# Kernel tuning notes

Hardware: AMD Instinct MI355X
Metric: run time of the kernel (lower is better)

## Reference

```python
import jax, jax.numpy as jnp
import numpy as np

N = 50000
E = 800000
NEG_SLOPE = 0.2
BN_EPS = 1e-5


def _gat_conv(x, src, dst, W, a_src, a_dst, bias, heads, out_ch, concat):
    # Linear projection per head: [N, heads, out_ch]
    h = (x @ W).reshape(-1, heads, out_ch)
    # Per-node attention terms alpha_src/alpha_dst: [N, heads]
    al_s = (h * a_src[None]).sum(-1)
    al_d = (h * a_dst[None]).sum(-1)
    # Edge logits with LeakyReLU: [E, heads]
    logits = jax.nn.leaky_relu(al_s[src] + al_d[dst], NEG_SLOPE)
    # Segment (scatter) softmax over edges grouped by destination node
    m = jax.ops.segment_max(logits, dst, num_segments=N)
    e = jnp.exp(logits - m[dst])
    s = jax.ops.segment_sum(e, dst, num_segments=N)
    alpha = e / (s[dst] + 1e-16)                      # [E, heads]
    # Weighted message aggregation: scatter-add to destinations
    msg = h[src] * alpha[:, :, None]                  # [E, heads, out_ch]
    out = jax.ops.segment_sum(msg, dst, num_segments=N)  # [N, heads, out_ch]
    out = out.reshape(-1, heads * out_ch) if concat else out.mean(axis=1)
    return out + bias


def _bn_eval(x, gamma, beta, mean, var):
    return (x - mean) * jax.lax.rsqrt(var + BN_EPS) * gamma + beta


def setup_inputs() -> dict:
    key = jax.random.key(0)
    ks = jax.random.split(key, 12)
    in_ch, hid, heads, out_cls = 128, 64, 2, 40
    return {
        "x": jax.random.normal(ks[0], (N, in_ch), jnp.float32),
        "edge_index": jax.random.randint(ks[1], (2, E), 0, N, jnp.int32),
        "W1": jax.random.normal(ks[2], (in_ch, heads * hid), jnp.float32) * 0.1,
        "a1_src": jax.random.normal(ks[3], (heads, hid), jnp.float32) * 0.1,
        "a1_dst": jax.random.normal(ks[4], (heads, hid), jnp.float32) * 0.1,
        "b1": jnp.zeros((heads * hid,), jnp.float32),
        "bn1_gamma": jnp.ones((heads * hid,), jnp.float32),
        "bn1_beta": jnp.zeros((heads * hid,), jnp.float32),
        "bn1_mean": jax.random.normal(ks[5], (heads * hid,), jnp.float32) * 0.1,
        "bn1_var": jax.random.uniform(ks[6], (heads * hid,), jnp.float32, 0.5, 1.5),
        "W2": jax.random.normal(ks[7], (heads * hid, out_cls), jnp.float32) * 0.1,
        "a2_src": jax.random.normal(ks[8], (1, out_cls), jnp.float32) * 0.1,
        "a2_dst": jax.random.normal(ks[9], (1, out_cls), jnp.float32) * 0.1,
        "b2": jnp.zeros((out_cls,), jnp.float32),
    }


def reference(x, edge_index, W1, a1_src, a1_dst, b1, bn1_gamma, bn1_beta,
              bn1_mean, bn1_var, W2, a2_src, a2_dst, b2):
    # add self loops
    loops = jnp.arange(N, dtype=edge_index.dtype)
    src = jnp.concatenate([edge_index[0], loops])
    dst = jnp.concatenate([edge_index[1], loops])
    # layer 1: GATConv(heads=2, concat) -> BN(eval) -> ReLU (dropout is eval no-op)
    h = _gat_conv(x, src, dst, W1, a1_src, a1_dst, b1, heads=2, out_ch=64, concat=True)
    h = jax.nn.relu(_bn_eval(h, bn1_gamma, bn1_beta, bn1_mean, bn1_var))
    # output layer: GATConv(heads=1, concat=False)
    out = _gat_conv(h, src, dst, W2, a2_src, a2_dst, b2, heads=1, out_ch=40, concat=False)
    return jax.nn.log_softmax(out, axis=1)
```

## Files before the change

kernel.cpp:

```cpp
#include <hip/hip_runtime.h>
#include <hip/hip_bf16.h>

#define NEG_SLOPE 0.2f
#define BN_EPS 1e-5f

#define NBLK 256
#define COARSE_SHIFT 9
#define COARSE_NPB 512

__device__ __forceinline__ float wred_sum(float v) {
    #pragma unroll
    for (int m = 32; m > 0; m >>= 1) v += __shfl_xor(v, m);
    return v;
}
__device__ __forceinline__ float wred_max(float v) {
    #pragma unroll
    for (int m = 32; m > 0; m >>= 1) v = fmaxf(v, __shfl_xor(v, m));
    return v;
}
__device__ __forceinline__ float xor16_sum(float v) {
    #pragma unroll
    for (int m = 1; m < 16; m <<= 1) v += __shfl_xor(v, m);
    return v;
}

__device__ __forceinline__ unsigned pack_bf16(float a, float b) {
    __hip_bfloat162 t;
    t.x = __float2bfloat16(a);
    t.y = __float2bfloat16(b);
    return *(unsigned*)&t;
}
__device__ __forceinline__ float2 unpack_bf16(unsigned u) {
    __hip_bfloat162 t = *(__hip_bfloat162*)&u;
    return {__bfloat162float(t.x), __bfloat162float(t.y)};
}

__device__ __forceinline__ unsigned enc_ord(float f) {
    unsigned u = __float_as_uint(f);
    return (u & 0x80000000u) ? ~u : (u | 0x80000000u);
}
__device__ __forceinline__ float dec_ord(unsigned e) {
    unsigned u = (e & 0x80000000u) ? (e ^ 0x80000000u) : ~e;
    return __uint_as_float(u);
}

__global__ __launch_bounds__(256) void part_hist(const int* __restrict__ ei, int E, int Et,
                                                 int chunk, int* __restrict__ hist, int nCoarse) {
    __shared__ int h[128];
    int b = blockIdx.x, t = threadIdx.x;
    if (t < 128) h[t] = 0;
    __syncthreads();
    int beg = b * chunk, end = min(beg + chunk, Et);
    for (int idx = beg + t; idx < end; idx += 256) {
        int d = (idx < E) ? ei[E + idx] : (idx - E);
        atomicAdd(&h[d >> COARSE_SHIFT], 1);
    }
    __syncthreads();
    if (t < nCoarse) hist[t * NBLK + b] = h[t];
}

__global__ __launch_bounds__(256) void coarse_total(const int* __restrict__ hist,
                                                    int* __restrict__ ctot) {
    __shared__ int red[256];
    int c = blockIdx.x, t = threadIdx.x;
    red[t] = hist[c * NBLK + t];
    __syncthreads();
    for (int off = 128; off > 0; off >>= 1) {
        if (t < off) red[t] += red[t + off];
        __syncthreads();
    }
    if (t == 0) ctot[c] = red[0];
}

__global__ __launch_bounds__(128) void coarse_scan(const int* __restrict__ ctot,
                                                   int* __restrict__ cbase, int nCoarse) {
    __shared__ int s[128];
    int t = threadIdx.x;
    int v = (t < nCoarse) ? ctot[t] : 0;
    s[t] = v;
    __syncthreads();
    for (int off = 1; off < 128; off <<= 1) {
        int u = (t >= off) ? s[t - off] : 0;
        __syncthreads();
        s[t] += u;
        __syncthreads();
    }
    if (t < nCoarse) cbase[t] = s[t] - v;
    if (t == 127) cbase[nCoarse] = s[127];
}

__global__ __launch_bounds__(64) void part_scan(int* __restrict__ hist,
                                                const int* __restrict__ cbase, int nCoarse) {
    int c = blockIdx.x, t = threadIdx.x;
    int base = cbase[c];
    int idx = c * NBLK + 4 * t;
    int4 v = *(int4*)&hist[idx];
    int sl = v.x + v.y + v.z + v.w;
    int inc = sl;
    #pragma unroll
    for (int off = 1; off < 64; off <<= 1) {
        int u = __shfl_up(inc, off);
        if (t >= off) inc += u;
    }
    int exc = inc - sl + base;
    int4 o;
    o.x = exc;
    o.y = exc + v.x;
    o.z = exc + v.x + v.y;
    o.w = exc + v.x + v.y + v.z;
    *(int4*)&hist[idx] = o;
}

__global__ __launch_bounds__(256) void part_scatter(const int* __restrict__ ei, int E, int Et,
                                                    int chunk, const int* __restrict__ hist,
                                                    unsigned* __restrict__ staged, int nCoarse) {
    __shared__ int cur[128];
    int b = blockIdx.x, t = threadIdx.x;
    if (t < nCoarse) cur[t] = hist[t * NBLK + b];
    __syncthreads();
    int beg = b * chunk, end = min(beg + chunk, Et);
    for (int idx = beg + t; idx < end; idx += 256) {
        int s, d;
        if (idx < E) { s = ei[idx]; d = ei[E + idx]; }
        else         { s = idx - E; d = idx - E; }
        int c = d >> COARSE_SHIFT;
        int pos = atomicAdd(&cur[c], 1);
        staged[pos] = ((unsigned)s << COARSE_SHIFT) | (unsigned)(d & (COARSE_NPB - 1));
    }
}

__global__ __launch_bounds__(512) void fine_place(const unsigned* __restrict__ staged,
                                                  const int* __restrict__ cbase,
                                                  int* __restrict__ offs,
                                                  int* __restrict__ csr, int Nn, int nCoarse) {
    __shared__ int hcnt[COARSE_NPB];
    __shared__ int scn[COARSE_NPB];
    int b = blockIdx.x, t = threadIdx.x;
    int node0 = b << COARSE_SHIFT;
    int nloc = min(COARSE_NPB, Nn - node0);
    hcnt[t] = 0;
    __syncthreads();
    int ebeg = cbase[b], eend = cbase[b + 1];
    for (int p = ebeg + t; p < eend; p += 512) {
        atomicAdd(&hcnt[staged[p] & (COARSE_NPB - 1)], 1);
    }
    __syncthreads();
    int val = hcnt[t];
    scn[t] = val;
    __syncthreads();
    for (int off = 1; off < COARSE_NPB; off <<= 1) {
        int u = (t >= off) ? scn[t - off] : 0;
        __syncthreads();
        scn[t] += u;
        __syncthreads();
    }
    int exc = ebeg + scn[t] - val;
    if (t < nloc) offs[node0 + t] = exc;
    if (b == nCoarse - 1 && t == 0) offs[Nn] = eend;
    hcnt[t] = exc;
    __syncthreads();
    for (int p = ebeg + t; p < eend; p += 512) {
        unsigned v = staged[p];
        int pos = atomicAdd(&hcnt[v & (COARSE_NPB - 1)], 1);
        csr[pos] = (int)(v >> COARSE_SHIFT);
    }
}

__global__ __launch_bounds__(256) void gemm1_tiled(const float* __restrict__ x,
                                                   const float* __restrict__ W,
                                                   const float* __restrict__ a1s,
                                                   const float* __restrict__ a1d,
                                                   unsigned* __restrict__ h1b,
                                                   float* __restrict__ als,
                                                   float* __restrict__ ald, int Nn) {
    __shared__ float Ast[32][132];
    __shared__ float Bs[32][132];
    int t  = threadIdx.x;
    int tx = t & 15;
    int ty = t >> 4;
    int br = blockIdx.x * 128;

    float acc[8][8];
    #pragma unroll
    for (int i = 0; i < 8; ++i)
        #pragma unroll
        for (int j = 0; j < 8; ++j) acc[i][j] = 0.f;

    int k4   = t & 7;
    int rowA = t >> 3;

    for (int k0 = 0; k0 < 128; k0 += 32) {
        #pragma unroll
        for (int i = 0; i < 4; ++i) {
            int r  = rowA + 32 * i;
            int gr = min(br + r, Nn - 1);
            float4 v = *(const float4*)(x + (size_t)gr * 128 + k0 + 4 * k4);
            Ast[4 * k4 + 0][r] = v.x; Ast[4 * k4 + 1][r] = v.y;
            Ast[4 * k4 + 2][r] = v.z; Ast[4 * k4 + 3][r] = v.w;
        }
        #pragma unroll
        for (int i = 0; i < 4; ++i) {
            int f  = t + 256 * i;
            int kk = f >> 5, c4 = f & 31;
            *(float4*)&Bs[kk][4 * c4] = *(const float4*)(W + (size_t)(k0 + kk) * 128 + 4 * c4);
        }
        __syncthreads();
        #pragma unroll 8
        for (int kk = 0; kk < 32; ++kk) {
            float4 a0 = *(const float4*)&Ast[kk][8 * ty];
            float4 a1 = *(const float4*)&Ast[kk][8 * ty + 4];
            float4 b0 = *(const float4*)&Bs[kk][8 * tx];
            float4 b1 = *(const float4*)&Bs[kk][8 * tx + 4];
            float av[8] = {a0.x, a0.y, a0.z, a0.w, a1.x, a1.y, a1.z, a1.w};
            float bv[8] = {b0.x, b0.y, b0.z, b0.w, b1.x, b1.y, b1.z, b1.w};
            #pragma unroll
            for (int i = 0; i < 8; ++i)
                #pragma unroll
                for (int j = 0; j < 8; ++j) acc[i][j] += av[i] * bv[j];
        }
        __syncthreads();
    }

    float a_s[8], a_d[8];
    #pragma unroll
    for (int j = 0; j < 8; ++j) { a_s[j] = a1s[8 * tx + j]; a_d[j] = a1d[8 * tx + j]; }
    bool h0 = (tx < 8);

    #pragma unroll
    for (int i = 0; i < 8; ++i) {
        int r = br + 8 * ty + i;
        if (r < Nn) {
            uint4 pk;
            pk.x = pack_bf16(acc[i][0], acc[i][1]);
            pk.y = pack_bf16(acc[i][2], acc[i][3]);
            pk.z = pack_bf16(acc[i][4], acc[i][5]);
            pk.w = pack_bf16(acc[i][6], acc[i][7]);
            *(uint4*)(h1b + (size_t)r * 64 + 4 * tx) = pk;
        }
        float ps = 0.f, pd = 0.f;
        #pragma unroll
        for (int j = 0; j < 8; ++j) { ps += acc[i][j] * a_s[j]; pd += acc[i][j] * a_d[j]; }
        float s0 = xor16_sum(h0 ? ps : 0.f);
        float s1 = xor16_sum(h0 ? 0.f : ps);
        float d0 = xor16_sum(h0 ? pd : 0.f);
        float d1 = xor16_sum(h0 ? 0.f : pd);
        if (tx == 0 && r < Nn) {
            als[r * 2] = s0; als[r * 2 + 1] = s1;
            ald[r * 2] = d0; ald[r * 2 + 1] = d1;
        }
    }
}

template <int H>
__global__ __launch_bounds__(256) void almax_kernel(const float* __restrict__ als,
                                                    unsigned* __restrict__ gmax,
                                                    int off, int Nn) {
    __shared__ float red[4][H];
    int t = threadIdx.x;
    float m[H];
    #pragma unroll
    for (int h = 0; h < H; ++h) m[h] = -1e30f;
    for (int n = blockIdx.x * 256 + t; n < Nn; n += gridDim.x * 256) {
        #pragma unroll
        for (int h = 0; h < H; ++h) m[h] = fmaxf(m[h], als[n * H + h]);
    }
    #pragma unroll
    for (int h = 0; h < H; ++h) m[h] = wred_max(m[h]);
    int wid = t >> 6;
    if ((t & 63) == 0) {
        #pragma unroll
        for (int h = 0; h < H; ++h) red[wid][h] = m[h];
    }
    __syncthreads();
    if (t == 0) {
        #pragma unroll
        for (int h = 0; h < H; ++h) {
            float mm = fmaxf(fmaxf(red[0][h], red[1][h]), fmaxf(red[2][h], red[3][h]));
            atomicMax(&gmax[off + h], enc_ord(mm));
        }
    }
}

__global__ __launch_bounds__(256) void softagg1_kernel(const int* __restrict__ offs, const int* __restrict__ csr,
                            const unsigned* __restrict__ h1b,
                            const float* __restrict__ als, const float* __restrict__ ald,
                            const unsigned* __restrict__ gmax,
                            const float* __restrict__ b1, const float* __restrict__ gam,
                            const float* __restrict__ bet, const float* __restrict__ mean,
                            const float* __restrict__ var, float* __restrict__ hbn, int Nn) {
    int wid = threadIdx.x >> 6, lane = threadIdx.x & 63;
    int n = blockIdx.x * 4 + wid;
    if (n >= Nn) return;
    int b = offs[n], e = offs[n + 1];
    int sub = lane >> 4;
    int l16 = lane & 15;
    int head = l16 >> 3;
    float aldh = ald[n * 2 + head];
    float bound = dec_ord(gmax[head]) + aldh;
    bound = (bound > 0.f) ? bound : NEG_SLOPE * bound;

    float acc[8];
    #pragma unroll
    for (int j = 0; j < 8; ++j) acc[j] = 0.f;
    float den = 0.f;
    for (int p = b + sub; p < e; p += 4) {
        int s = csr[p];
        float al = als[s * 2 + head] + aldh;
        al = (al > 0.f) ? al : NEG_SLOPE * al;
        float ev = __expf(al - bound);
        uint4 v = *(const uint4*)(h1b + (size_t)s * 64 + 4 * l16);
        float2 f0 = unpack_bf16(v.x), f1 = unpack_bf16(v.y);
        float2 f2 = unpack_bf16(v.z), f3 = unpack_bf16(v.w);
        acc[0] += f0.x * ev; acc[1] += f0.y * ev;
        acc[2] += f1.x * ev; acc[3] += f1.y * ev;
        acc[4] += f2.x * ev; acc[5] += f2.y * ev;
        acc[6] += f3.x * ev; acc[7] += f3.y * ev;
        den += ev;
    }
    #pragma unroll
    for (int j = 0; j < 8; ++j) {
        acc[j] += __shfl_xor(acc[j], 16);
        acc[j] += __shfl_xor(acc[j], 32);
    }
    den += __shfl_xor(den, 16);
    den += __shfl_xor(den, 32);
    if (sub == 0) {
        float inv = 1.f / (den + 1e-16f);
        int c = 8 * l16;
        #pragma unroll
        for (int half = 0; half < 2; ++half) {
            int cc = c + 4 * half;
            float4 bb = *(const float4*)(b1 + cc);
            float4 gg = *(const float4*)(gam + cc);
            float4 be = *(const float4*)(bet + cc);
            float4 mm = *(const float4*)(mean + cc);
            float4 vv = *(const float4*)(var + cc);
            float4 o;
            o.x = fmaxf((acc[4*half+0] * inv + bb.x - mm.x) * rsqrtf(vv.x + BN_EPS) * gg.x + be.x, 0.f);
            o.y = fmaxf((acc[4*half+1] * inv + bb.y - mm.y) * rsqrtf(vv.y + BN_EPS) * gg.y + be.y, 0.f);
            o.z = fmaxf((acc[4*half+2] * inv + bb.z - mm.z) * rsqrtf(vv.z + BN_EPS) * gg.z + be.z, 0.f);
            o.w = fmaxf((acc[4*half+3] * inv + bb.w - mm.w) * rsqrtf(vv.w + BN_EPS) * gg.w + be.w, 0.f);
            *(float4*)(hbn + (size_t)n * 128 + cc) = o;
        }
    }
}

__global__ __launch_bounds__(256) void gemm2_tiled(const float* __restrict__ hbn,
                                                   const float* __restrict__ W2,
                                                   const float* __restrict__ a2s,
                                                   const float* __restrict__ a2d,
                                                   unsigned* __restrict__ h2b,
                                                   float* __restrict__ als, float* __restrict__ ald,
                                                   int Nn) {
    __shared__ float Ast[32][132];
    __shared__ float Bs[32][68];
    int t  = threadIdx.x;
    int tx = t & 15;
    int ty = t >> 4;
    int br = blockIdx.x * 128;

    float as4[4], ad4[4];
    #pragma unroll
    for (int j = 0; j < 4; ++j) {
        int c = 4 * tx + j;
        as4[j] = (c < 40) ? a2s[c] : 0.f;
        ad4[j] = (c < 40) ? a2d[c] : 0.f;
    }

    float acc[8][4];
    #pragma unroll
    for (int i = 0; i < 8; ++i)
        #pragma unroll
        for (int j = 0; j < 4; ++j) acc[i][j] = 0.f;

    int k4   = t & 7;
    int rowA = t >> 3;

    for (int k0 = 0; k0 < 128; k0 += 32) {
        #pragma unroll
        for (int i = 0; i < 4; ++i) {
            int r  = rowA + 32 * i;
            int gr = min(br + r, Nn - 1);
            float4 v = *(const float4*)(hbn + (size_t)gr * 128 + k0 + 4 * k4);
            Ast[4 * k4 + 0][r] = v.x; Ast[4 * k4 + 1][r] = v.y;
            Ast[4 * k4 + 2][r] = v.z; Ast[4 * k4 + 3][r] = v.w;
        }
        #pragma unroll
        for (int i = 0; i < 2; ++i) {
            int f  = t + 256 * i;
            int kk = f >> 4, c4 = f & 15;
            float4 v = {0.f, 0.f, 0.f, 0.f};
            if (c4 < 10) v = *(const float4*)(W2 + (size_t)(k0 + kk) * 40 + 4 * c4);
            *(float4*)&Bs[kk][4 * c4] = v;
        }
        __syncthreads();
        #pragma unroll 8
        for (int kk = 0; kk < 32; ++kk) {
            float4 a0 = *(const float4*)&Ast[kk][8 * ty];
            float4 a1 = *(const float4*)&Ast[kk][8 * ty + 4];
            float4 b0 = *(const float4*)&Bs[kk][4 * tx];
            float av[8] = {a0.x, a0.y, a0.z, a0.w, a1.x, a1.y, a1.z, a1.w};
            #pragma unroll
            for (int i = 0; i < 8; ++i) {
                acc[i][0] += av[i] * b0.x; acc[i][1] += av[i] * b0.y;
                acc[i][2] += av[i] * b0.z; acc[i][3] += av[i] * b0.w;
            }
        }
        __syncthreads();
    }

    #pragma unroll
    for (int i = 0; i < 8; ++i) {
        int r = br + 8 * ty + i;
        if (r < Nn) {
            uint2 pk = {pack_bf16(acc[i][0], acc[i][1]), pack_bf16(acc[i][2], acc[i][3])};
            *(uint2*)(h2b + (size_t)r * 32 + 2 * tx) = pk;
        }
        float ps = acc[i][0] * as4[0] + acc[i][1] * as4[1] + acc[i][2] * as4[2] + acc[i][3] * as4[3];
        float pd = acc[i][0] * ad4[0] + acc[i][1] * ad4[1] + acc[i][2] * ad4[2] + acc[i][3] * ad4[3];
        float sS = xor16_sum(ps);
        float sD = xor16_sum(pd);
        if (tx == 0 && r < Nn) { als[r] = sS; ald[r] = sD; }
    }
}

__global__ __launch_bounds__(256) void softagg2_kernel(const int* __restrict__ offs, const int* __restrict__ csr,
                            const unsigned* __restrict__ h2b,
                            const float* __restrict__ als, const float* __restrict__ ald,
                            const unsigned* __restrict__ gmax,
                            const float* __restrict__ b2,
                            float* __restrict__ out, int Nn) {
    int wid = threadIdx.x >> 6, lane = threadIdx.x & 63;
    int n = blockIdx.x * 4 + wid;
    if (n >= Nn) return;
    int b = offs[n], e = offs[n + 1];
    float aldn = ald[n];
    float bound = dec_ord(gmax[2]) + aldn;
    bound = (bound > 0.f) ? bound : NEG_SLOPE * bound;

    int sub = lane >> 4;
    int l16 = lane & 15;
    float acc[4];
    #pragma unroll
    for (int j = 0; j < 4; ++j) acc[j] = 0.f;
    float den = 0.f;
    for (int p = b + sub; p < e; p += 4) {
        int s = csr[p];
        float l = als[s] + aldn;
        l = (l > 0.f) ? l : NEG_SLOPE * l;
        float ev = __expf(l - bound);
        uint2 v = *(const uint2*)(h2b + (size_t)s * 32 + 2 * l16);
        float2 f0 = unpack_bf16(v.x), f1 = unpack_bf16(v.y);
        acc[0] += f0.x * ev; acc[1] += f0.y * ev;
        acc[2] += f1.x * ev; acc[3] += f1.y * ev;
        den += ev;
    }
    #pragma unroll
    for (int j = 0; j < 4; ++j) {
        acc[j] += __shfl_xor(acc[j], 16);
        acc[j] += __shfl_xor(acc[j], 32);
    }
    den += __shfl_xor(den, 16);
    den += __shfl_xor(den, 32);
    float inv = 1.f / (den + 1e-16f);
    bool valid = (l16 < 10);
    float v0 = -1e30f, v1 = -1e30f, v2 = -1e30f, v3 = -1e30f;
    if (valid) {
        int c = 4 * l16;
        v0 = acc[0] * inv + b2[c];
        v1 = acc[1] * inv + b2[c + 1];
        v2 = acc[2] * inv + b2[c + 2];
        v3 = acc[3] * inv + b2[c + 3];
    }
    float m = wred_max(fmaxf(fmaxf(v0, v1), fmaxf(v2, v3)));
    float es = (valid && sub == 0)
             ? (__expf(v0 - m) + __expf(v1 - m) + __expf(v2 - m) + __expf(v3 - m)) : 0.f;
    float ssum = wred_sum(es);
    float lse = m + logf(ssum);
    if (sub == 0 && valid) {
        float4 o = {v0 - lse, v1 - lse, v2 - lse, v3 - lse};
        *(float4*)(out + (size_t)n * 40 + 4 * l16) = o;
    }
}

extern "C" void kernel_launch(void* const* d_in, const int* in_sizes, int n_in,
                              void* d_out, int out_size, void* d_ws, size_t ws_size,
                              hipStream_t stream) {
    const float* x    = (const float*)d_in[0];
    const int*   ei   = (const int*)d_in[1];
    const float* W1   = (const float*)d_in[2];
    const float* a1s  = (const float*)d_in[3];
    const float* a1d  = (const float*)d_in[4];
    const float* b1   = (const float*)d_in[5];
    const float* g1   = (const float*)d_in[6];
    const float* be1  = (const float*)d_in[7];
    const float* mn1  = (const float*)d_in[8];
    const float* vr1  = (const float*)d_in[9];
    const float* W2   = (const float*)d_in[10];
    const float* a2s  = (const float*)d_in[11];
    const float* a2d  = (const float*)d_in[12];
    const float* b2   = (const float*)d_in[13];
    float* out = (float*)d_out;

    const int N  = in_sizes[0] / 128;
    const int E  = in_sizes[1] / 2;
    const int Et = E + N;
    const int nCoarse = (N + COARSE_NPB - 1) >> COARSE_SHIFT;
    const int chunk   = (Et + NBLK - 1) / NBLK;

    char* p = (char*)d_ws;
    auto alloc = [&](size_t bytes) -> void* {
        void* r = (void*)p;
        p += (bytes + 255) & ~(size_t)255;
        return r;
    };
    int*      hist   = (int*)alloc((size_t)nCoarse * NBLK * 4);
    int*      ctot   = (int*)alloc((size_t)nCoarse * 4);
    int*      cbase  = (int*)alloc((size_t)(nCoarse + 1) * 4);
    int*      offs   = (int*)alloc((size_t)(N + 1) * 4);
    unsigned* staged = (unsigned*)alloc((size_t)Et * 4);
    int*      csr    = (int*)alloc((size_t)Et * 4);
    unsigned* h1b    = (unsigned*)alloc((size_t)N * 64 * 4);
    float*    al1sv  = (float*)alloc((size_t)N * 2 * 4);
    float*    al1dv  = (float*)alloc((size_t)N * 2 * 4);
    float*    hbn    = (float*)alloc((size_t)N * 128 * 4);
    unsigned* h2b    = (unsigned*)alloc((size_t)N * 32 * 4);
    float*    al2sv  = (float*)alloc((size_t)N * 4);
    float*    al2dv  = (float*)alloc((size_t)N * 4);
    unsigned* gmax   = (unsigned*)alloc(4 * 4);
    (void)ws_size;

    hipMemsetAsync(gmax, 0, 16, stream);

    part_hist<<<NBLK, 256, 0, stream>>>(ei, E, Et, chunk, hist, nCoarse);
    coarse_total<<<nCoarse, 256, 0, stream>>>(hist, ctot);
    coarse_scan<<<1, 128, 0, stream>>>(ctot, cbase, nCoarse);
    part_scan<<<nCoarse, 64, 0, stream>>>(hist, cbase, nCoarse);
    part_scatter<<<NBLK, 256, 0, stream>>>(ei, E, Et, chunk, hist, staged, nCoarse);
    fine_place<<<nCoarse, 512, 0, stream>>>(staged, cbase, offs, csr, N, nCoarse);

    gemm1_tiled<<<(N + 127) / 128, 256, 0, stream>>>(x, W1, a1s, a1d, h1b, al1sv, al1dv, N);
    almax_kernel<2><<<64, 256, 0, stream>>>(al1sv, gmax, 0, N);
    softagg1_kernel<<<(N + 3) / 4, 256, 0, stream>>>(offs, csr, h1b, al1sv, al1dv, gmax,
                                                     b1, g1, be1, mn1, vr1, hbn, N);

    gemm2_tiled<<<(N + 127) / 128, 256, 0, stream>>>(hbn, W2, a2s, a2d, h2b, al2sv, al2dv, N);
    almax_kernel<1><<<64, 256, 0, stream>>>(al2sv, gmax, 2, N);
    softagg2_kernel<<<(N + 3) / 4, 256, 0, stream>>>(offs, csr, h2b, al2sv, al2dv, gmax, b2, out, N);
}
```

Measured before the change: 267.6 us.

## Stage edge batches in LDS and widen edge parallelism in softmax aggregation

Both aggregation kernels now load up to 64 incoming edges per wave cooperatively, one edge per lane. Each lane computes that edge's attention exponent once and stages the source index and weight in shared memory. Groups of 8 lanes then gather feature rows for 8 edges at a time, instead of 4, using wider vector loads. This removes the redundant per-lane index and exponent work and puts more gathers in flight. Separately, the BatchNorm scale and shift are folded once in the max-reduction kernel, which shortens the epilogue. The cost is extra LDS traffic, more accumulator registers, and reliance on a wave not needing a barrier between its own LDS write and read.

New measurement: 262.8 us. No clear change (-1.8%).

```diff
diff --git a/kernel.cpp b/kernel.cpp
--- a/kernel.cpp
+++ b/kernel.cpp
@@ -253,10 +253,21 @@
 
 template <int H>
 __global__ __launch_bounds__(256) void almax_kernel(const float* __restrict__ als,
-                                                    unsigned* __restrict__ gmax,
-                                                    int off, int Nn) {
+                                                    unsigned* __restrict__ gmax, int off, int Nn,
+                                                    const float* __restrict__ b1,
+                                                    const float* __restrict__ g1,
+                                                    const float* __restrict__ be1,
+                                                    const float* __restrict__ mn1,
+                                                    const float* __restrict__ vr1,
+                                                    float* __restrict__ bnscale,
+                                                    float* __restrict__ bnshift) {
     __shared__ float red[4][H];
     int t = threadIdx.x;
+    if (bnscale && blockIdx.x == 0 && t < 128) {
+        float sc = rsqrtf(vr1[t] + BN_EPS) * g1[t];
+        bnscale[t] = sc;
+        bnshift[t] = be1[t] + (b1[t] - mn1[t]) * sc;
+    }
     float m[H];
     #pragma unroll
     for (int h = 0; h < H; ++h) m[h] = -1e30f;
@@ -285,63 +296,97 @@
                             const unsigned* __restrict__ h1b,
                             const float* __restrict__ als, const float* __restrict__ ald,
                             const unsigned* __restrict__ gmax,
-                            const float* __restrict__ b1, const float* __restrict__ gam,
-                            const float* __restrict__ bet, const float* __restrict__ mean,
-                            const float* __restrict__ var, float* __restrict__ hbn, int Nn) {
+                            const float* __restrict__ bnscale, const float* __restrict__ bnshift,
+                            float* __restrict__ hbn, int Nn) {
+    __shared__ int   sh_s[4][64];
+    __shared__ float sh_e0[4][64];
+    __shared__ float sh_e1[4][64];
     int wid = threadIdx.x >> 6, lane = threadIdx.x & 63;
     int n = blockIdx.x * 4 + wid;
     if (n >= Nn) return;
     int b = offs[n], e = offs[n + 1];
-    int sub = lane >> 4;
-    int l16 = lane & 15;
-    int head = l16 >> 3;
-    float aldh = ald[n * 2 + head];
-    float bound = dec_ord(gmax[head]) + aldh;
-    bound = (bound > 0.f) ? bound : NEG_SLOPE * bound;
-
-    float acc[8];
-    #pragma unroll
-    for (int j = 0; j < 8; ++j) acc[j] = 0.f;
-    float den = 0.f;
-    for (int p = b + sub; p < e; p += 4) {
-        int s = csr[p];
-        float al = als[s * 2 + head] + aldh;
-        al = (al > 0.f) ? al : NEG_SLOPE * al;
-        float ev = __expf(al - bound);
-        uint4 v = *(const uint4*)(h1b + (size_t)s * 64 + 4 * l16);
-        float2 f0 = unpack_bf16(v.x), f1 = unpack_bf16(v.y);
-        float2 f2 = unpack_bf16(v.z), f3 = unpack_bf16(v.w);
-        acc[0] += f0.x * ev; acc[1] += f0.y * ev;
-        acc[2] += f1.x * ev; acc[3] += f1.y * ev;
-        acc[4] += f2.x * ev; acc[5] += f2.y * ev;
-        acc[6] += f3.x * ev; acc[7] += f3.y * ev;
-        den += ev;
-    }
-    #pragma unroll
-    for (int j = 0; j < 8; ++j) {
+    float2 aldn = *(const float2*)(ald + n * 2);
+    float bd0 = dec_ord(gmax[0]) + aldn.x; bd0 = (bd0 > 0.f) ? bd0 : NEG_SLOPE * bd0;
+    float bd1 = dec_ord(gmax[1]) + aldn.y; bd1 = (bd1 > 0.f) ? bd1 : NEG_SLOPE * bd1;
+
+    int eslot = lane >> 3;
+    int l8    = lane & 7;
+    float acc[16];
+    #pragma unroll
+    for (int j = 0; j < 16; ++j) acc[j] = 0.f;
+    float den0 = 0.f, den1 = 0.f;
+
+    for (int base = b; base < e; base += 64) {
+        int cnt = min(64, e - base);
+        int   s1 = 0;
+        float e0r = 0.f, e1r = 0.f;
+        if (lane < cnt) {
+            s1 = csr[base + lane];
+            float2 as = *(const float2*)(als + (size_t)s1 * 2);
+            float l0 = as.x + aldn.x; l0 = (l0 > 0.f) ? l0 : NEG_SLOPE * l0;
+            float l1 = as.y + aldn.y; l1 = (l1 > 0.f) ? l1 : NEG_SLOPE * l1;
+            e0r = __expf(l0 - bd0);
+            e1r = __expf(l1 - bd1);
+            den0 += e0r; den1 += e1r;
+        }
+        sh_s[wid][lane]  = s1;
+        sh_e0[wid][lane] = e0r;
+        sh_e1[wid][lane] = e1r;
+        for (int i = eslot; i < cnt; i += 8) {
+            int   s  = sh_s[wid][i];
+            float e0 = sh_e0[wid][i];
+            float e1 = sh_e1[wid][i];
+            uint4 va = *(const uint4*)(h1b + (size_t)s * 64 + 4 * l8);
+            uint4 vb = *(const uint4*)(h1b + (size_t)s * 64 + 32 + 4 * l8);
+            float2 f;
+            f = unpack_bf16(va.x); acc[0]  += f.x * e0; acc[1]  += f.y * e0;
+            f = unpack_bf16(va.y); acc[2]  += f.x * e0; acc[3]  += f.y * e0;
+            f = unpack_bf16(va.z); acc[4]  += f.x * e0; acc[5]  += f.y * e0;
+            f = unpack_bf16(va.w); acc[6]  += f.x * e0; acc[7]  += f.y * e0;
+            f = unpack_bf16(vb.x); acc[8]  += f.x * e1; acc[9]  += f.y * e1;
+            f = unpack_bf16(vb.y); acc[10] += f.x * e1; acc[11] += f.y * e1;
+            f = unpack_bf16(vb.z); acc[12] += f.x * e1; acc[13] += f.y * e1;
+            f = unpack_bf16(vb.w); acc[14] += f.x * e1; acc[15] += f.y * e1;
+        }
+    }
+    #pragma unroll
+    for (int j = 0; j < 16; ++j) {
+        acc[j] += __shfl_xor(acc[j], 8);
         acc[j] += __shfl_xor(acc[j], 16);
         acc[j] += __shfl_xor(acc[j], 32);
     }
-    den += __shfl_xor(den, 16);
-    den += __shfl_xor(den, 32);
-    if (sub == 0) {
-        float inv = 1.f / (den + 1e-16f);
-        int c = 8 * l16;
-        #pragma unroll
-        for (int half = 0; half < 2; ++half) {
-            int cc = c + 4 * half;
-            float4 bb = *(const float4*)(b1 + cc);
-            float4 gg = *(const float4*)(gam + cc);
-            float4 be = *(const float4*)(bet + cc);
-            float4 mm = *(const float4*)(mean + cc);
-            float4 vv = *(const float4*)(var + cc);
-            float4 o;
-            o.x = fmaxf((acc[4*half+0] * inv + bb.x - mm.x) * rsqrtf(vv.x + BN_EPS) * gg.x + be.x, 0.f);
-            o.y = fmaxf((acc[4*half+1] * inv + bb.y - mm.y) * rsqrtf(vv.y + BN_EPS) * gg.y + be.y, 0.f);
-            o.z = fmaxf((acc[4*half+2] * inv + bb.z - mm.z) * rsqrtf(vv.z + BN_EPS) * gg.z + be.z, 0.f);
-            o.w = fmaxf((acc[4*half+3] * inv + bb.w - mm.w) * rsqrtf(vv.w + BN_EPS) * gg.w + be.w, 0.f);
-            *(float4*)(hbn + (size_t)n * 128 + cc) = o;
-        }
+    den0 = wred_sum(den0);
+    den1 = wred_sum(den1);
+    if (eslot == 0) {
+        float inv0 = 1.f / (den0 + 1e-16f);
+        float inv1 = 1.f / (den1 + 1e-16f);
+        int c0 = 8 * l8, c1 = 64 + 8 * l8;
+        float4 sa = *(const float4*)(bnscale + c0), sb = *(const float4*)(bnscale + c0 + 4);
+        float4 ha = *(const float4*)(bnshift + c0), hb = *(const float4*)(bnshift + c0 + 4);
+        float4 oa, ob;
+        oa.x = fmaxf(acc[0] * inv0 * sa.x + ha.x, 0.f);
+        oa.y = fmaxf(acc[1] * inv0 * sa.y + ha.y, 0.f);
+        oa.z = fmaxf(acc[2] * inv0 * sa.z + ha.z, 0.f);
+        oa.w = fmaxf(acc[3] * inv0 * sa.w + ha.w, 0.f);
+        ob.x = fmaxf(acc[4] * inv0 * sb.x + hb.x, 0.f);
+        ob.y = fmaxf(acc[5] * inv0 * sb.y + hb.y, 0.f);
+        ob.z = fmaxf(acc[6] * inv0 * sb.z + hb.z, 0.f);
+        ob.w = fmaxf(acc[7] * inv0 * sb.w + hb.w, 0.f);
+        *(float4*)(hbn + (size_t)n * 128 + c0)     = oa;
+        *(float4*)(hbn + (size_t)n * 128 + c0 + 4) = ob;
+        float4 sc = *(const float4*)(bnscale + c1), sd = *(const float4*)(bnscale + c1 + 4);
+        float4 hc = *(const float4*)(bnshift + c1), hd = *(const float4*)(bnshift + c1 + 4);
+        float4 oc, od;
+        oc.x = fmaxf(acc[8]  * inv1 * sc.x + hc.x, 0.f);
+        oc.y = fmaxf(acc[9]  * inv1 * sc.y + hc.y, 0.f);
+        oc.z = fmaxf(acc[10] * inv1 * sc.z + hc.z, 0.f);
+        oc.w = fmaxf(acc[11] * inv1 * sc.w + hc.w, 0.f);
+        od.x = fmaxf(acc[12] * inv1 * sd.x + hd.x, 0.f);
+        od.y = fmaxf(acc[13] * inv1 * sd.y + hd.y, 0.f);
+        od.z = fmaxf(acc[14] * inv1 * sd.z + hd.z, 0.f);
+        od.w = fmaxf(acc[15] * inv1 * sd.w + hd.w, 0.f);
+        *(float4*)(hbn + (size_t)n * 128 + c1)     = oc;
+        *(float4*)(hbn + (size_t)n * 128 + c1 + 4) = od;
     }
 }
 
@@ -430,6 +475,8 @@
                             const unsigned* __restrict__ gmax,
                             const float* __restrict__ b2,
                             float* __restrict__ out, int Nn) {
+    __shared__ int   sh_s[4][64];
+    __shared__ float sh_ev[4][64];
     int wid = threadIdx.x >> 6, lane = threadIdx.x & 63;
     int n = blockIdx.x * 4 + wid;
     if (n >= Nn) return;
@@ -438,48 +485,69 @@
     float bound = dec_ord(gmax[2]) + aldn;
     bound = (bound > 0.f) ? bound : NEG_SLOPE * bound;
 
-    int sub = lane >> 4;
-    int l16 = lane & 15;
-    float acc[4];
-    #pragma unroll
-    for (int j = 0; j < 4; ++j) acc[j] = 0.f;
+    int eslot = lane >> 3;
+    int l8    = lane & 7;
+    float acc[8];
+    #pragma unroll
+    for (int j = 0; j < 8; ++j) acc[j] = 0.f;
     float den = 0.f;
-    for (int p = b + sub; p < e; p += 4) {
-        int s = csr[p];
-        float l = als[s] + aldn;
-        l = (l > 0.f) ? l : NEG_SLOPE * l;
-        float ev = __expf(l - bound);
-        uint2 v = *(const uint2*)(h2b + (size_t)s * 32 + 2 * l16);
-        float2 f0 = unpack_bf16(v.x), f1 = unpack_bf16(v.y);
-        acc[0] += f0.x * ev; acc[1] += f0.y * ev;
-        acc[2] += f1.x * ev; acc[3] += f1.y * ev;
-        den += ev;
-    }
-    #pragma unroll
-    for (int j = 0; j < 4; ++j) {
+
+    for (int base = b; base < e; base += 64) {
+        int cnt = min(64, e - base);
+        int   s1 = 0;
+        float evr = 0.f;
+        if (lane < cnt) {
+            s1 = csr[base + lane];
+            float l = als[s1] + aldn;
+            l = (l > 0.f) ? l : NEG_SLOPE * l;
+            evr = __expf(l - bound);
+            den += evr;
+        }
+        sh_s[wid][lane]  = s1;
+        sh_ev[wid][lane] = evr;
+        for (int i = eslot; i < cnt; i += 8) {
+            int   s  = sh_s[wid][i];
+            float ev = sh_ev[wid][i];
+            uint4 v = *(const uint4*)(h2b + (size_t)s * 32 + 4 * l8);
+            float2 f;
+            f = unpack_bf16(v.x); acc[0] += f.x * ev; acc[1] += f.y * ev;
+            f = unpack_bf16(v.y); acc[2] += f.x * ev; acc[3] += f.y * ev;
+            f = unpack_bf16(v.z); acc[4] += f.x * ev; acc[5] += f.y * ev;
+            f = unpack_bf16(v.w); acc[6] += f.x * ev; acc[7] += f.y * ev;
+        }
+    }
+    #pragma unroll
+    for (int j = 0; j < 8; ++j) {
+        acc[j] += __shfl_xor(acc[j], 8);
         acc[j] += __shfl_xor(acc[j], 16);
         acc[j] += __shfl_xor(acc[j], 32);
     }
-    den += __shfl_xor(den, 16);
-    den += __shfl_xor(den, 32);
+    den = wred_sum(den);
     float inv = 1.f / (den + 1e-16f);
-    bool valid = (l16 < 10);
-    float v0 = -1e30f, v1 = -1e30f, v2 = -1e30f, v3 = -1e30f;
+    bool valid = (eslot == 0) && (l8 < 5);
+    float vv[8];
+    float lmax = -1e30f;
     if (valid) {
-        int c = 4 * l16;
-        v0 = acc[0] * inv + b2[c];
-        v1 = acc[1] * inv + b2[c + 1];
-        v2 = acc[2] * inv + b2[c + 2];
-        v3 = acc[3] * inv + b2[c + 3];
-    }
-    float m = wred_max(fmaxf(fmaxf(v0, v1), fmaxf(v2, v3)));
-    float es = (valid && sub == 0)
-             ? (__expf(v0 - m) + __expf(v1 - m) + __expf(v2 - m) + __expf(v3 - m)) : 0.f;
+        int c = 8 * l8;
+        #pragma unroll
+        for (int j = 0; j < 8; ++j) {
+            vv[j] = acc[j] * inv + b2[c + j];
+            lmax = fmaxf(lmax, vv[j]);
+        }
+    }
+    float m = wred_max(lmax);
+    float es = 0.f;
+    if (valid) {
+        #pragma unroll
+        for (int j = 0; j < 8; ++j) es += __expf(vv[j] - m);
+    }
     float ssum = wred_sum(es);
     float lse = m + logf(ssum);
-    if (sub == 0 && valid) {
-        float4 o = {v0 - lse, v1 - lse, v2 - lse, v3 - lse};
-        *(float4*)(out + (size_t)n * 40 + 4 * l16) = o;
+    if (valid) {
+        float4 oa = {vv[0] - lse, vv[1] - lse, vv[2] - lse, vv[3] - lse};
+        float4 ob = {vv[4] - lse, vv[5] - lse, vv[6] - lse, vv[7] - lse};
+        *(float4*)(out + (size_t)n * 40 + 8 * l8)     = oa;
+        *(float4*)(out + (size_t)n * 40 + 8 * l8 + 4) = ob;
     }
 }
 
@@ -528,6 +596,8 @@
     float*    al2sv  = (float*)alloc((size_t)N * 4);
     float*    al2dv  = (float*)alloc((size_t)N * 4);
     unsigned* gmax   = (unsigned*)alloc(4 * 4);
+    float*    bnscale= (float*)alloc(128 * 4);
+    float*    bnshift= (float*)alloc(128 * 4);
     (void)ws_size;
 
     hipMemsetAsync(gmax, 0, 16, stream);
@@ -540,11 +610,12 @@
     fine_place<<<nCoarse, 512, 0, stream>>>(staged, cbase, offs, csr, N, nCoarse);
 
     gemm1_tiled<<<(N + 127) / 128, 256, 0, stream>>>(x, W1, a1s, a1d, h1b, al1sv, al1dv, N);
-    almax_kernel<2><<<64, 256, 0, stream>>>(al1sv, gmax, 0, N);
+    almax_kernel<2><<<64, 256, 0, stream>>>(al1sv, gmax, 0, N, b1, g1, be1, mn1, vr1, bnscale, bnshift);
     softagg1_kernel<<<(N + 3) / 4, 256, 0, stream>>>(offs, csr, h1b, al1sv, al1dv, gmax,
-                                                     b1, g1, be1, mn1, vr1, hbn, N);
+                                                     bnscale, bnshift, hbn, N);
 
     gemm2_tiled<<<(N + 127) / 128, 256, 0, stream>>>(hbn, W2, a2s, a2d, h2b, al2sv, al2dv, N);
-    almax_kernel<1><<<64, 256, 0, stream>>>(al2sv, gmax, 2, N);
+    almax_kernel<1><<<64, 256, 0, stream>>>(al2sv, gmax, 2, N, nullptr, nullptr, nullptr, nullptr,
+                                            nullptr, nullptr, nullptr);
     softagg2_kernel<<<(N + 3) / 4, 256, 0, stream>>>(offs, csr, h2b, al2sv, al2dv, gmax, b2, out, N);
 }
```
